# Kernel optimization log

Measured on AMD Instinct MI355X. Metric: run time of the kernel, lower is better.

Reference implementation:

```python
import jax, jax.numpy as jnp
import numpy as np

B, T, I, H, O = 64, 2048, 256, 256, 128

def _rnn_scan(xp, W_hh):
    # xp: [T, B, H] = precomputed W_ih @ x + b_ih + b_hh per timestep
    h0 = jnp.zeros((xp.shape[1], W_hh.shape[0]), xp.dtype)
    def step(h, xt):
        h_new = jnp.tanh(xt + h @ W_hh.T)
        return h_new, h_new
    _, hs = jax.lax.scan(step, h0, xp)
    return hs  # [T, B, H]

def setup_inputs() -> dict:
    key = jax.random.key(0)
    ks = jax.random.split(key, 9)
    s1 = 1.0 / np.sqrt(H)
    s2 = 1.0 / np.sqrt(O)
    return {
        "x": jax.random.normal(ks[0], (B, T, I), dtype=jnp.float32),
        "W_ih1": jax.random.normal(ks[1], (H, I), dtype=jnp.float32) * s1,
        "W_hh1": jax.random.normal(ks[2], (H, H), dtype=jnp.float32) * s1,
        "b_ih1": jax.random.normal(ks[3], (H,), dtype=jnp.float32) * s1,
        "b_hh1": jax.random.normal(ks[4], (H,), dtype=jnp.float32) * s1,
        "W_ih2": jax.random.normal(ks[5], (O, H), dtype=jnp.float32) * s2,
        "W_hh2": jax.random.normal(ks[6], (O, O), dtype=jnp.float32) * s2,
        "b_ih2": jax.random.normal(ks[7], (O,), dtype=jnp.float32) * s2,
        "b_hh2": jax.random.normal(ks[8], (O,), dtype=jnp.float32) * s2,
    }

def reference(x, W_ih1, W_hh1, b_ih1, b_hh1, W_ih2, W_hh2, b_ih2, b_hh2):
    # Layer 1: h_t = tanh(W_ih1 x_t + b_ih1 + W_hh1 h_{t-1} + b_hh1)
    xp1 = jnp.einsum('bti,hi->tbh', x, W_ih1) + (b_ih1 + b_hh1)
    h1 = _rnn_scan(xp1, W_hh1)                      # [T, B, H]
    # Layer 2: o_t = tanh(W_ih2 h_t + b_ih2 + W_hh2 o_{t-1} + b_hh2)
    xp2 = jnp.einsum('tbh,oh->tbo', h1, W_ih2) + (b_ih2 + b_hh2)
    h2 = _rnn_scan(xp2, W_hh2)                      # [T, B, O]
    out = jnp.transpose(h2, (1, 0, 2)).reshape(-1, O)  # [B*T, num_classes]
    return out
```

## Files before the change

### kernel.cpp

```cpp
#include <hip/hip_runtime.h>
#include <math.h>

#define BB 64
#define TT 2048
#define II 256
#define HH 256
#define OO 128

template<int N>
__global__ __launch_bounds__(256)
void gemm_bias(const float* __restrict__ A, const float* __restrict__ W,
               const float* __restrict__ b1, const float* __restrict__ b2,
               float* __restrict__ C)
{
    constexpr int K = 256;
    __shared__ float sA[16][132];
    __shared__ float sB[16][132];
    const int tid  = threadIdx.x;
    const long row0 = (long)blockIdx.x * 128;
    const int  col0 = blockIdx.y * 128;

    const int tm = tid & 15;
    const int tn = tid >> 4;

    float acc[8][8];
#pragma unroll
    for (int i = 0; i < 8; ++i)
#pragma unroll
        for (int j = 0; j < 8; ++j) acc[i][j] = 0.f;

    const int f0  = tid;
    const int f1  = tid + 256;
    const int am0 = f0 >> 2, ak0 = (f0 & 3) * 4;
    const int am1 = f1 >> 2, ak1 = (f1 & 3) * 4;

    for (int kt = 0; kt < K; kt += 16) {
        float4 a0 = *(const float4*)&A[(row0 + am0) * K + kt + ak0];
        float4 a1 = *(const float4*)&A[(row0 + am1) * K + kt + ak1];
        float4 w0 = *(const float4*)&W[(long)(col0 + am0) * K + kt + ak0];
        float4 w1 = *(const float4*)&W[(long)(col0 + am1) * K + kt + ak1];
        __syncthreads();
        sA[ak0+0][am0] = a0.x; sA[ak0+1][am0] = a0.y; sA[ak0+2][am0] = a0.z; sA[ak0+3][am0] = a0.w;
        sA[ak1+0][am1] = a1.x; sA[ak1+1][am1] = a1.y; sA[ak1+2][am1] = a1.z; sA[ak1+3][am1] = a1.w;
        sB[ak0+0][am0] = w0.x; sB[ak0+1][am0] = w0.y; sB[ak0+2][am0] = w0.z; sB[ak0+3][am0] = w0.w;
        sB[ak1+0][am1] = w1.x; sB[ak1+1][am1] = w1.y; sB[ak1+2][am1] = w1.z; sB[ak1+3][am1] = w1.w;
        __syncthreads();
#pragma unroll
        for (int k = 0; k < 16; ++k) {
            float4 av0 = *(const float4*)&sA[k][tm * 8];
            float4 av1 = *(const float4*)&sA[k][tm * 8 + 4];
            float4 bv0 = *(const float4*)&sB[k][tn * 8];
            float4 bv1 = *(const float4*)&sB[k][tn * 8 + 4];
            float am[8] = {av0.x, av0.y, av0.z, av0.w, av1.x, av1.y, av1.z, av1.w};
            float bn[8] = {bv0.x, bv0.y, bv0.z, bv0.w, bv1.x, bv1.y, bv1.z, bv1.w};
#pragma unroll
            for (int i = 0; i < 8; ++i)
#pragma unroll
                for (int j = 0; j < 8; ++j)
                    acc[i][j] += am[i] * bn[j];
        }
    }

    float bias[8];
#pragma unroll
    for (int j = 0; j < 8; ++j) {
        int col = col0 + tn * 8 + j;
        bias[j] = b1[col] + b2[col];
    }
#pragma unroll
    for (int i = 0; i < 8; ++i) {
        long row = row0 + tm * 8 + i;
        float4 v0, v1;
        v0.x = acc[i][0] + bias[0]; v0.y = acc[i][1] + bias[1];
        v0.z = acc[i][2] + bias[2]; v0.w = acc[i][3] + bias[3];
        v1.x = acc[i][4] + bias[4]; v1.y = acc[i][5] + bias[5];
        v1.z = acc[i][6] + bias[6]; v1.w = acc[i][7] + bias[7];
        *(float4*)&C[row * N + col0 + tn * 8]     = v0;
        *(float4*)&C[row * N + col0 + tn * 8 + 4] = v1;
    }
}

__device__ __forceinline__ float fast_tanh(float x) {
    float e = __expf(2.f * x);
    return 1.f - 2.f / (e + 1.f);
}

__global__ __launch_bounds__(512, 2)
void rnn_pipe(const float* __restrict__ W_hh1,
              const float* __restrict__ W_ih2,
              const float* __restrict__ W_hh2,
              const float* __restrict__ b_ih2,
              const float* __restrict__ b_hh2,
              float* __restrict__ XH,
              float* __restrict__ out,
              int* __restrict__ flags)
{
    const int tid = threadIdx.x;
    const int g   = tid & 31;
    const int ks  = tid >> 5;

    if (blockIdx.x < BB) {
        __shared__ float h_lds[256];
        __shared__ float part[16 * 256];
        const int b = blockIdx.x;

        float4 w[8][4];
#pragma unroll
        for (int r = 0; r < 8; ++r)
#pragma unroll
            for (int c = 0; c < 4; ++c)
                w[r][c] = *(const float4*)&W_hh1[(g * 8 + r) * 256 + ks * 16 + c * 4];

        float* rowp = XH + (long)b * TT * HH;
        float xp = 0.f;
        if (tid < 256) {
            h_lds[tid] = 0.f;
            xp = rowp[tid];
        }
        __syncthreads();

        for (int t = 0; t < TT; ++t) {
            float4 h4[4];
#pragma unroll
            for (int c = 0; c < 4; ++c)
                h4[c] = *(const float4*)&h_lds[ks * 16 + c * 4];

            float acc[8];
#pragma unroll
            for (int r = 0; r < 8; ++r) acc[r] = 0.f;
#pragma unroll
            for (int c = 0; c < 4; ++c)
#pragma unroll
                for (int r = 0; r < 8; ++r)
                    acc[r] += w[r][c].x * h4[c].x + w[r][c].y * h4[c].y
                            + w[r][c].z * h4[c].z + w[r][c].w * h4[c].w;

            *(float4*)&part[ks * 256 + g * 8]     = make_float4(acc[0], acc[1], acc[2], acc[3]);
            *(float4*)&part[ks * 256 + g * 8 + 4] = make_float4(acc[4], acc[5], acc[6], acc[7]);
            __syncthreads();

            if (tid < 256) {
                float s0 = part[0 * 256 + tid] + part[1 * 256 + tid]
                         + part[2 * 256 + tid] + part[3 * 256 + tid];
                float s1 = part[4 * 256 + tid] + part[5 * 256 + tid]
                         + part[6 * 256 + tid] + part[7 * 256 + tid];
                float s2 = part[8 * 256 + tid] + part[9 * 256 + tid]
                         + part[10 * 256 + tid] + part[11 * 256 + tid];
                float s3 = part[12 * 256 + tid] + part[13 * 256 + tid]
                         + part[14 * 256 + tid] + part[15 * 256 + tid];
                float v = fast_tanh(((s0 + s1) + (s2 + s3)) + xp);
                h_lds[tid] = v;
                rowp[(long)t * HH + tid] = v;
                if (t + 1 < TT) xp = rowp[(long)(t + 1) * HH + tid];
            }
            __syncthreads();

            if ((t & 3) == 3 && tid == 0)
                __hip_atomic_store(&flags[b], t + 1, __ATOMIC_RELEASE,
                                   __HIP_MEMORY_SCOPE_AGENT);
        }
    } else {
        __shared__ float h1_lds[256];
        __shared__ float o_lds[128];
        __shared__ float part2[16 * 132];
        const int b = blockIdx.x - BB;

        float4 wi[4][4];
        float4 wh[4][2];
#pragma unroll
        for (int r = 0; r < 4; ++r) {
#pragma unroll
            for (int c = 0; c < 4; ++c)
                wi[r][c] = *(const float4*)&W_ih2[(g * 4 + r) * 256 + ks * 16 + c * 4];
#pragma unroll
            for (int c = 0; c < 2; ++c)
                wh[r][c] = *(const float4*)&W_hh2[(g * 4 + r) * 128 + ks * 8 + c * 4];
        }

        float bias = 0.f;
        if (tid < 128) {
            bias = b_ih2[tid] + b_hh2[tid];
            o_lds[tid] = 0.f;
        }
        const float* h1p = XH + (long)b * TT * HH;
        float* outp      = out + (long)b * TT * OO;
        __syncthreads();

        int seen = 0;
        for (int t = 0; t < TT; ++t) {
            if (seen <= t) {
                do {
                    seen = __hip_atomic_load(&flags[b], __ATOMIC_ACQUIRE,
                                             __HIP_MEMORY_SCOPE_AGENT);
                } while (seen <= t);
            }
            if (tid < 64)
                *(float4*)&h1_lds[tid * 4] = *(const float4*)&h1p[(long)t * HH + tid * 4];
            __syncthreads();

            float4 h4[4];
#pragma unroll
            for (int c = 0; c < 4; ++c)
                h4[c] = *(const float4*)&h1_lds[ks * 16 + c * 4];
            float4 o4[2];
#pragma unroll
            for (int c = 0; c < 2; ++c)
                o4[c] = *(const float4*)&o_lds[ks * 8 + c * 4];

            float acc[4];
#pragma unroll
            for (int r = 0; r < 4; ++r) acc[r] = 0.f;
#pragma unroll
            for (int c = 0; c < 4; ++c)
#pragma unroll
                for (int r = 0; r < 4; ++r)
                    acc[r] += wi[r][c].x * h4[c].x + wi[r][c].y * h4[c].y
                            + wi[r][c].z * h4[c].z + wi[r][c].w * h4[c].w;
#pragma unroll
            for (int c = 0; c < 2; ++c)
#pragma unroll
                for (int r = 0; r < 4; ++r)
                    acc[r] += wh[r][c].x * o4[c].x + wh[r][c].y * o4[c].y
                            + wh[r][c].z * o4[c].z + wh[r][c].w * o4[c].w;

            *(float4*)&part2[ks * 132 + g * 4] = make_float4(acc[0], acc[1], acc[2], acc[3]);
            __syncthreads();

            if (tid < 128) {
                float s = bias;
#pragma unroll
                for (int s16 = 0; s16 < 16; ++s16)
                    s += part2[s16 * 132 + tid];
                float v = fast_tanh(s);
                o_lds[tid] = v;
                outp[(long)t * OO + tid] = v;
            }
        }
    }
}

extern "C" void kernel_launch(void* const* d_in, const int* in_sizes, int n_in,
                              void* d_out, int out_size, void* d_ws, size_t ws_size,
                              hipStream_t stream)
{
    const float* x     = (const float*)d_in[0];
    const float* W_ih1 = (const float*)d_in[1];
    const float* W_hh1 = (const float*)d_in[2];
    const float* b_ih1 = (const float*)d_in[3];
    const float* b_hh1 = (const float*)d_in[4];
    const float* W_ih2 = (const float*)d_in[5];
    const float* W_hh2 = (const float*)d_in[6];
    const float* b_ih2 = (const float*)d_in[7];
    const float* b_hh2 = (const float*)d_in[8];
    float* out = (float*)d_out;

    float* xp1 = (float*)d_ws;
    const size_t FLAG_OFF = (size_t)BB * TT * HH * sizeof(float);
    int* flags = (int*)((char*)d_ws + FLAG_OFF);

    const int M = BB * TT;

    hipMemsetAsync(flags, 0, BB * sizeof(int), stream);

    dim3 gA(M / 128, HH / 128);
    gemm_bias<HH><<<gA, 256, 0, stream>>>(x, W_ih1, b_ih1, b_hh1, xp1);

    rnn_pipe<<<2 * BB, 512, 0, stream>>>(W_hh1, W_ih2, W_hh2, b_ih2, b_hh2,
                                         xp1, out, flags);
}
```

Measured before the change: 2.066 ms.

## Batch recurrent steps across 16 sequences per block using fp16 MFMA

Rewrites both recurrent layers so that each block handles 16 batch rows and computes each timestep as a small matrix product with fp16 MFMA. Before, each block handled one sequence with scalar FMAs and an LDS reduction. The projection GEMM now writes its output time-major so a block can load its 16 rows contiguously. Layer-1 hidden states are stored as fp16 in place in the workspace, flag updates are batched every 8 steps, and layer 2 prefetches the next h1 tile when it is already available. The rewrite cuts the launch from 128 blocks to 8 and reduces hidden-state and weight precision to fp16, which risks accuracy drift over 2048 steps.

```diff
diff --git a/kernel.cpp b/kernel.cpp
--- a/kernel.cpp
+++ b/kernel.cpp
@@ -7,13 +7,20 @@
 #define HH 256
 #define OO 128
 
-template<int N>
+typedef _Float16 half8 __attribute__((ext_vector_type(8)));
+typedef float floatx4 __attribute__((ext_vector_type(4)));
+
+__device__ __forceinline__ float fast_tanh(float x) {
+    float e = __expf(2.f * x);
+    return 1.f - 2.f / (e + 1.f);
+}
+
 __global__ __launch_bounds__(256)
-void gemm_bias(const float* __restrict__ A, const float* __restrict__ W,
-               const float* __restrict__ b1, const float* __restrict__ b2,
-               float* __restrict__ C)
+void gemm_bias_T(const float* __restrict__ A, const float* __restrict__ W,
+                 const float* __restrict__ b1, const float* __restrict__ b2,
+                 float* __restrict__ C)
 {
-    constexpr int K = 256;
+    constexpr int K = 256, N = 256;
     __shared__ float sA[16][132];
     __shared__ float sB[16][132];
     const int tid  = threadIdx.x;
@@ -69,171 +76,219 @@
     }
 #pragma unroll
     for (int i = 0; i < 8; ++i) {
-        long row = row0 + tm * 8 + i;
+        long row  = row0 + tm * 8 + i;
+        long bidx = row >> 11;
+        long tidx = row & 2047;
+        float* op = &C[(tidx * BB + bidx) * 256 + col0 + tn * 8];
         float4 v0, v1;
         v0.x = acc[i][0] + bias[0]; v0.y = acc[i][1] + bias[1];
         v0.z = acc[i][2] + bias[2]; v0.w = acc[i][3] + bias[3];
         v1.x = acc[i][4] + bias[4]; v1.y = acc[i][5] + bias[5];
         v1.z = acc[i][6] + bias[6]; v1.w = acc[i][7] + bias[7];
-        *(float4*)&C[row * N + col0 + tn * 8]     = v0;
-        *(float4*)&C[row * N + col0 + tn * 8 + 4] = v1;
+        *(float4*)op       = v0;
+        *(float4*)(op + 4) = v1;
     }
 }
 
-__device__ __forceinline__ float fast_tanh(float x) {
-    float e = __expf(2.f * x);
-    return 1.f - 2.f / (e + 1.f);
-}
-
-__global__ __launch_bounds__(512, 2)
+__global__ __launch_bounds__(256, 1)
 void rnn_pipe(const float* __restrict__ W_hh1,
               const float* __restrict__ W_ih2,
               const float* __restrict__ W_hh2,
               const float* __restrict__ b_ih2,
               const float* __restrict__ b_hh2,
-              float* __restrict__ XH,
+              float* __restrict__ XP,
               float* __restrict__ out,
               int* __restrict__ flags)
 {
-    const int tid = threadIdx.x;
-    const int g   = tid & 31;
-    const int ks  = tid >> 5;
-
-    if (blockIdx.x < BB) {
-        __shared__ float h_lds[256];
-        __shared__ float part[16 * 256];
-        const int b = blockIdx.x;
-
-        float4 w[8][4];
-#pragma unroll
-        for (int r = 0; r < 8; ++r)
-#pragma unroll
-            for (int c = 0; c < 4; ++c)
-                w[r][c] = *(const float4*)&W_hh1[(g * 8 + r) * 256 + ks * 16 + c * 4];
-
-        float* rowp = XH + (long)b * TT * HH;
-        float xp = 0.f;
-        if (tid < 256) {
-            h_lds[tid] = 0.f;
-            xp = rowp[tid];
+    const int tid  = threadIdx.x;
+    const int wave = tid >> 6;
+    const int lane = tid & 63;
+    const int q    = lane >> 4;
+    const int l15  = lane & 15;
+
+    if (blockIdx.x < 4) {
+        const int p  = blockIdx.x;
+        const int m0 = p * 16;
+        const int n0 = wave * 64;
+        __shared__ _Float16 hbuf[16 * 264];
+
+        half8 bf[4][8];
+#pragma unroll
+        for (int j = 0; j < 4; ++j)
+#pragma unroll
+            for (int s = 0; s < 8; ++s) {
+                const float* wp = W_hh1 + (long)(n0 + j * 16 + l15) * 256 + s * 32 + q * 8;
+                float4 u0 = *(const float4*)wp;
+                float4 u1 = *(const float4*)(wp + 4);
+                half8 h;
+                h[0] = (_Float16)u0.x; h[1] = (_Float16)u0.y;
+                h[2] = (_Float16)u0.z; h[3] = (_Float16)u0.w;
+                h[4] = (_Float16)u1.x; h[5] = (_Float16)u1.y;
+                h[6] = (_Float16)u1.z; h[7] = (_Float16)u1.w;
+                bf[j][s] = h;
+            }
+
+        for (int i = tid; i < 16 * 264; i += 256) hbuf[i] = (_Float16)0.f;
+
+        float xpn[4][4];
+#pragma unroll
+        for (int j = 0; j < 4; ++j)
+#pragma unroll
+            for (int i = 0; i < 4; ++i)
+                xpn[j][i] = XP[((long)0 * BB + m0 + q * 4 + i) * 256 + n0 + j * 16 + l15];
+        __syncthreads();
+
+        for (int t = 0; t < TT; ++t) {
+            half8 a[8];
+#pragma unroll
+            for (int s = 0; s < 8; ++s)
+                a[s] = *(const half8*)&hbuf[l15 * 264 + s * 32 + q * 8];
+
+            floatx4 c[4] = {{0.f,0.f,0.f,0.f},{0.f,0.f,0.f,0.f},
+                            {0.f,0.f,0.f,0.f},{0.f,0.f,0.f,0.f}};
+#pragma unroll
+            for (int s = 0; s < 8; ++s)
+#pragma unroll
+                for (int j = 0; j < 4; ++j)
+                    c[j] = __builtin_amdgcn_mfma_f32_16x16x32_f16(a[s], bf[j][s], c[j], 0, 0, 0);
+
+            __syncthreads();
+
+            if ((t & 7) == 0 && t > 0 && tid == 0)
+                __hip_atomic_store(&flags[p], t, __ATOMIC_RELEASE,
+                                   __HIP_MEMORY_SCOPE_AGENT);
+
+#pragma unroll
+            for (int j = 0; j < 4; ++j)
+#pragma unroll
+                for (int i = 0; i < 4; ++i) {
+                    float v = fast_tanh(c[j][i] + xpn[j][i]);
+                    hbuf[(q * 4 + i) * 264 + n0 + j * 16 + l15] = (_Float16)v;
+                }
+            __syncthreads();
+
+            {
+                const int r   = tid >> 4;
+                const int o16 = (tid & 15) * 16;
+                half8 v0 = *(const half8*)&hbuf[r * 264 + o16];
+                half8 v1 = *(const half8*)&hbuf[r * 264 + o16 + 8];
+                _Float16* gp = (_Float16*)(XP + ((long)t * BB + m0 + r) * 256) + o16;
+                *(half8*)gp       = v0;
+                *(half8*)(gp + 8) = v1;
+            }
+            if (t + 1 < TT) {
+#pragma unroll
+                for (int j = 0; j < 4; ++j)
+#pragma unroll
+                    for (int i = 0; i < 4; ++i)
+                        xpn[j][i] = XP[((long)(t + 1) * BB + m0 + q * 4 + i) * 256
+                                       + n0 + j * 16 + l15];
+            }
         }
         __syncthreads();
+        if (tid == 0)
+            __hip_atomic_store(&flags[p], TT, __ATOMIC_RELEASE,
+                               __HIP_MEMORY_SCOPE_AGENT);
+    } else {
+        const int p  = blockIdx.x - 4;
+        const int m0 = p * 16;
+        const int n0 = wave * 32;
+        __shared__ _Float16 obuf[16 * 136];
+
+        half8 bf1[2][8];
+        half8 bf2[2][4];
+#pragma unroll
+        for (int j = 0; j < 2; ++j) {
+#pragma unroll
+            for (int s = 0; s < 8; ++s) {
+                const float* wp = W_ih2 + (long)(n0 + j * 16 + l15) * 256 + s * 32 + q * 8;
+                float4 u0 = *(const float4*)wp;
+                float4 u1 = *(const float4*)(wp + 4);
+                half8 h;
+                h[0] = (_Float16)u0.x; h[1] = (_Float16)u0.y;
+                h[2] = (_Float16)u0.z; h[3] = (_Float16)u0.w;
+                h[4] = (_Float16)u1.x; h[5] = (_Float16)u1.y;
+                h[6] = (_Float16)u1.z; h[7] = (_Float16)u1.w;
+                bf1[j][s] = h;
+            }
+#pragma unroll
+            for (int s = 0; s < 4; ++s) {
+                const float* wp = W_hh2 + (long)(n0 + j * 16 + l15) * 128 + s * 32 + q * 8;
+                float4 u0 = *(const float4*)wp;
+                float4 u1 = *(const float4*)(wp + 4);
+                half8 h;
+                h[0] = (_Float16)u0.x; h[1] = (_Float16)u0.y;
+                h[2] = (_Float16)u0.z; h[3] = (_Float16)u0.w;
+                h[4] = (_Float16)u1.x; h[5] = (_Float16)u1.y;
+                h[6] = (_Float16)u1.z; h[7] = (_Float16)u1.w;
+                bf2[j][s] = h;
+            }
+        }
+
+        float bias[2];
+#pragma unroll
+        for (int j = 0; j < 2; ++j)
+            bias[j] = b_ih2[n0 + j * 16 + l15] + b_hh2[n0 + j * 16 + l15];
+
+        for (int i = tid; i < 16 * 136; i += 256) obuf[i] = (_Float16)0.f;
+        __syncthreads();
+
+        int seen = 0;
+        bool have = false;
+        half8 a1[8];
 
         for (int t = 0; t < TT; ++t) {
-            float4 h4[4];
-#pragma unroll
-            for (int c = 0; c < 4; ++c)
-                h4[c] = *(const float4*)&h_lds[ks * 16 + c * 4];
-
-            float acc[8];
-#pragma unroll
-            for (int r = 0; r < 8; ++r) acc[r] = 0.f;
-#pragma unroll
-            for (int c = 0; c < 4; ++c)
-#pragma unroll
-                for (int r = 0; r < 8; ++r)
-                    acc[r] += w[r][c].x * h4[c].x + w[r][c].y * h4[c].y
-                            + w[r][c].z * h4[c].z + w[r][c].w * h4[c].w;
-
-            *(float4*)&part[ks * 256 + g * 8]     = make_float4(acc[0], acc[1], acc[2], acc[3]);
-            *(float4*)&part[ks * 256 + g * 8 + 4] = make_float4(acc[4], acc[5], acc[6], acc[7]);
+            if (!have) {
+                if (seen <= t) {
+                    do {
+                        seen = __hip_atomic_load(&flags[p], __ATOMIC_ACQUIRE,
+                                                 __HIP_MEMORY_SCOPE_AGENT);
+                    } while (seen <= t);
+                }
+                const _Float16* h1p =
+                    (const _Float16*)(XP + ((long)t * BB + m0 + l15) * 256);
+#pragma unroll
+                for (int s = 0; s < 8; ++s)
+                    a1[s] = *(const half8*)(h1p + s * 32 + q * 8);
+            }
+
+            half8 a2[4];
+#pragma unroll
+            for (int s = 0; s < 4; ++s)
+                a2[s] = *(const half8*)&obuf[l15 * 136 + s * 32 + q * 8];
+
+            floatx4 c[2] = {{0.f,0.f,0.f,0.f},{0.f,0.f,0.f,0.f}};
+#pragma unroll
+            for (int s = 0; s < 8; ++s)
+#pragma unroll
+                for (int j = 0; j < 2; ++j)
+                    c[j] = __builtin_amdgcn_mfma_f32_16x16x32_f16(a1[s], bf1[j][s], c[j], 0, 0, 0);
+#pragma unroll
+            for (int s = 0; s < 4; ++s)
+#pragma unroll
+                for (int j = 0; j < 2; ++j)
+                    c[j] = __builtin_amdgcn_mfma_f32_16x16x32_f16(a2[s], bf2[j][s], c[j], 0, 0, 0);
+
             __syncthreads();
 
-            if (tid < 256) {
-                float s0 = part[0 * 256 + tid] + part[1 * 256 + tid]
-                         + part[2 * 256 + tid] + part[3 * 256 + tid];
-                float s1 = part[4 * 256 + tid] + part[5 * 256 + tid]
-                         + part[6 * 256 + tid] + part[7 * 256 + tid];
-                float s2 = part[8 * 256 + tid] + part[9 * 256 + tid]
-                         + part[10 * 256 + tid] + part[11 * 256 + tid];
-                float s3 = part[12 * 256 + tid] + part[13 * 256 + tid]
-                         + part[14 * 256 + tid] + part[15 * 256 + tid];
-                float v = fast_tanh(((s0 + s1) + (s2 + s3)) + xp);
-                h_lds[tid] = v;
-                rowp[(long)t * HH + tid] = v;
-                if (t + 1 < TT) xp = rowp[(long)(t + 1) * HH + tid];
-            }
+#pragma unroll
+            for (int j = 0; j < 2; ++j)
+#pragma unroll
+                for (int i = 0; i < 4; ++i) {
+                    float v = fast_tanh(c[j][i] + bias[j]);
+                    obuf[(q * 4 + i) * 136 + n0 + j * 16 + l15] = (_Float16)v;
+                    out[((long)(m0 + q * 4 + i) * TT + t) * OO + n0 + j * 16 + l15] = v;
+                }
             __syncthreads();
 
-            if ((t & 3) == 3 && tid == 0)
-                __hip_atomic_store(&flags[b], t + 1, __ATOMIC_RELEASE,
-                                   __HIP_MEMORY_SCOPE_AGENT);
-        }
-    } else {
-        __shared__ float h1_lds[256];
-        __shared__ float o_lds[128];
-        __shared__ float part2[16 * 132];
-        const int b = blockIdx.x - BB;
-
-        float4 wi[4][4];
-        float4 wh[4][2];
-#pragma unroll
-        for (int r = 0; r < 4; ++r) {
-#pragma unroll
-            for (int c = 0; c < 4; ++c)
-                wi[r][c] = *(const float4*)&W_ih2[(g * 4 + r) * 256 + ks * 16 + c * 4];
-#pragma unroll
-            for (int c = 0; c < 2; ++c)
-                wh[r][c] = *(const float4*)&W_hh2[(g * 4 + r) * 128 + ks * 8 + c * 4];
-        }
-
-        float bias = 0.f;
-        if (tid < 128) {
-            bias = b_ih2[tid] + b_hh2[tid];
-            o_lds[tid] = 0.f;
-        }
-        const float* h1p = XH + (long)b * TT * HH;
-        float* outp      = out + (long)b * TT * OO;
-        __syncthreads();
-
-        int seen = 0;
-        for (int t = 0; t < TT; ++t) {
-            if (seen <= t) {
-                do {
-                    seen = __hip_atomic_load(&flags[b], __ATOMIC_ACQUIRE,
-                                             __HIP_MEMORY_SCOPE_AGENT);
-                } while (seen <= t);
-            }
-            if (tid < 64)
-                *(float4*)&h1_lds[tid * 4] = *(const float4*)&h1p[(long)t * HH + tid * 4];
-            __syncthreads();
-
-            float4 h4[4];
-#pragma unroll
-            for (int c = 0; c < 4; ++c)
-                h4[c] = *(const float4*)&h1_lds[ks * 16 + c * 4];
-            float4 o4[2];
-#pragma unroll
-            for (int c = 0; c < 2; ++c)
-                o4[c] = *(const float4*)&o_lds[ks * 8 + c * 4];
-
-            float acc[4];
-#pragma unroll
-            for (int r = 0; r < 4; ++r) acc[r] = 0.f;
-#pragma unroll
-            for (int c = 0; c < 4; ++c)
-#pragma unroll
-                for (int r = 0; r < 4; ++r)
-                    acc[r] += wi[r][c].x * h4[c].x + wi[r][c].y * h4[c].y
-                            + wi[r][c].z * h4[c].z + wi[r][c].w * h4[c].w;
-#pragma unroll
-            for (int c = 0; c < 2; ++c)
-#pragma unroll
-                for (int r = 0; r < 4; ++r)
-                    acc[r] += wh[r][c].x * o4[c].x + wh[r][c].y * o4[c].y
-                            + wh[r][c].z * o4[c].z + wh[r][c].w * o4[c].w;
-
-            *(float4*)&part2[ks * 132 + g * 4] = make_float4(acc[0], acc[1], acc[2], acc[3]);
-            __syncthreads();
-
-            if (tid < 128) {
-                float s = bias;
-#pragma unroll
-                for (int s16 = 0; s16 < 16; ++s16)
-                    s += part2[s16 * 132 + tid];
-                float v = fast_tanh(s);
-                o_lds[tid] = v;
-                outp[(long)t * OO + tid] = v;
+            have = false;
+            if (t + 1 < TT && seen > t + 1) {
+                const _Float16* h1p =
+                    (const _Float16*)(XP + ((long)(t + 1) * BB + m0 + l15) * 256);
+#pragma unroll
+                for (int s = 0; s < 8; ++s)
+                    a1[s] = *(const half8*)(h1p + s * 32 + q * 8);
+                have = true;
             }
         }
     }
@@ -254,17 +309,15 @@
     const float* b_hh2 = (const float*)d_in[8];
     float* out = (float*)d_out;
 
-    float* xp1 = (float*)d_ws;
-    const size_t FLAG_OFF = (size_t)BB * TT * HH * sizeof(float);
+    float* xpT = (float*)d_ws;
+    const size_t FLAG_OFF = (size_t)TT * BB * HH * sizeof(float);
     int* flags = (int*)((char*)d_ws + FLAG_OFF);
 
-    const int M = BB * TT;
-
-    hipMemsetAsync(flags, 0, BB * sizeof(int), stream);
-
-    dim3 gA(M / 128, HH / 128);
-    gemm_bias<HH><<<gA, 256, 0, stream>>>(x, W_ih1, b_ih1, b_hh1, xp1);
-
-    rnn_pipe<<<2 * BB, 512, 0, stream>>>(W_hh1, W_ih2, W_hh2, b_ih2, b_hh2,
-                                         xp1, out, flags);
+    hipMemsetAsync(flags, 0, 4 * sizeof(int), stream);
+
+    dim3 gA(BB * TT / 128, HH / 128);
+    gemm_bias_T<<<gA, 256, 0, stream>>>(x, W_ih1, b_ih1, b_hh1, xpT);
+
+    rnn_pipe<<<8, 256, 0, stream>>>(W_hh1, W_ih2, W_hh2, b_ih2, b_hh2,
+                                    xpT, out, flags);
 }
```

After: 3.815 ms. 1.85x slower.
